# Optimization experiments

Hardware: AMD Instinct MI355X
Metric: run time of the kernel (lower is better)

The kernel has to match this reference:

```python
import jax, jax.numpy as jnp
import numpy as np

EPS = 1e-08
LAMBDA_SIM = 1.0
LAMBDA_SPARSITY = 0.001
B, D, K = 8192, 4096, 64


def setup_inputs() -> dict:
    key = jax.random.key(0)
    k1, k2, k3, k4, k5 = jax.random.split(key, 5)
    labels = jax.random.randint(k1, (B,), 0, K)
    hard_class_probs = jax.nn.one_hot(labels, K, dtype=jnp.float32)  # [B,K] hard one-hot
    return {
        "hard_class_probs": hard_class_probs,
        "masked_activations_1b": jax.random.normal(k2, (B, D), dtype=jnp.float32),
        "masked_activations_8b": jax.random.normal(k3, (B, D), dtype=jnp.float32),
        "mask_1b": jax.random.uniform(k4, (B, D), dtype=jnp.float32),
        "mask_8b": jax.random.uniform(k5, (B, D), dtype=jnp.float32),
    }


def _classwise_pairwise_cossim(acts, hard_class_probs):
    # F.normalize(p=2, dim=-1, eps=EPS): x / max(||x||, eps)
    norms = jnp.sqrt(jnp.sum(acts * acts, axis=-1, keepdims=True))
    norm_acts = acts / jnp.maximum(norms, EPS)                      # [B,D]
    S = norm_acts @ norm_acts.T                                      # [B,B] gram of unit vectors
    diag = jnp.sum(norm_acts * norm_acts, axis=-1)                   # [B] (== diag(S))
    M = (hard_class_probs > 0.5).astype(acts.dtype)                  # [B,K] hard membership
    n = jnp.sum(M, axis=0)                                           # [K] class counts
    SM = S @ M                                                       # [B,K]
    mSm = jnp.sum(M * SM, axis=0)                                    # [K] sum_{i,j in class} S_ij
    sum_diag = M.T @ diag                                            # [K]
    pair_sum = 0.5 * (mSm - sum_diag)                                # sum over i<j pairs
    n_pairs = 0.5 * n * (n - 1.0)
    valid = n >= 2.0
    per_class_mean = jnp.where(valid, pair_sum / jnp.maximum(n_pairs, 1.0), 0.0)
    n_valid = jnp.sum(valid.astype(acts.dtype))
    return jnp.where(n_valid > 0, jnp.sum(per_class_mean) / jnp.maximum(n_valid, 1.0), 0.0)


def _binary_entropy(p):
    p = jnp.clip(p, EPS, 1.0 - EPS)
    return jnp.mean(-(p * jnp.log(p) + (1.0 - p) * jnp.log(1.0 - p)))


def _combined_loss(hard_class_probs, masked_activations, mask):
    sim_loss = -_classwise_pairwise_cossim(masked_activations, hard_class_probs)
    sparsity_loss = _binary_entropy(mask)
    total = LAMBDA_SIM * sim_loss + LAMBDA_SPARSITY * sparsity_loss
    return total, sim_loss, sparsity_loss


def reference(hard_class_probs, masked_activations_1b, masked_activations_8b, mask_1b, mask_8b):
    loss_1b, sim_1b, sp_1b = _combined_loss(hard_class_probs, masked_activations_1b, mask_1b)
    loss_8b, sim_8b, sp_8b = _combined_loss(hard_class_probs, masked_activations_8b, mask_8b)
    total_loss = loss_1b + loss_8b
    return (total_loss, sim_1b, sim_8b, sp_1b, sp_8b)
```

## Files before the change

### kernel.cpp

```cpp
#include <hip/hip_runtime.h>
#include <math.h>

#define B_ 8192
#define D_ 4096
#define K_ 64
#define EPSF 1e-8f
#define NSPLIT 4
#define LN2F 0.69314718056f

#define ENT_GRID 2048
#define ENT_BLOCK 256

typedef float f32x4 __attribute__((ext_vector_type(4)));


__device__ __forceinline__ float wave_reduce_f(float v) {
#pragma unroll
  for (int o = 32; o > 0; o >>= 1) v += __shfl_down(v, o);
  return v;
}


__global__ void k_init(int* __restrict__ counts) {
  if (threadIdx.x < K_) counts[threadIdx.x] = 0;
}

__global__ void k_labels(const float* __restrict__ probs, int* __restrict__ labels,
                         int* __restrict__ counts, int* __restrict__ rowlist) {
  int row = blockIdx.x * 4 + (threadIdx.x >> 6);
  int lane = threadIdx.x & 63;
  float p = probs[(size_t)row * K_ + lane];
  unsigned long long m = __ballot(p > 0.5f);
  if (lane == 0) {
    int k = __ffsll(m) - 1;
    if (k >= 0) {
      labels[row] = k;
      int pos = atomicAdd(&counts[k], 1);
      rowlist[k * B_ + pos] = row;
    }
  }
}

__device__ __forceinline__ float ent1(float p) {
  p = fminf(fmaxf(p, EPSF), 1.0f - EPSF);
  float q = 1.0f - p;
  float lp = __builtin_amdgcn_logf(p);
  float lq = __builtin_amdgcn_logf(fmaxf(q, 1e-38f));
  return -(p * lp + q * lq);
}

__device__ __forceinline__ float ent4(f32x4 v) {
  return ent1(v.x) + ent1(v.y) + ent1(v.z) + ent1(v.w);
}

__global__ __launch_bounds__(ENT_BLOCK) void k_entropy(const f32x4* __restrict__ m1,
                                                       const f32x4* __restrict__ m8,
                                                       double* __restrict__ entpart) {
  __shared__ float lds[8];
  const int NTH = ENT_GRID * ENT_BLOCK;
  int tid = blockIdx.x * ENT_BLOCK + threadIdx.x;
  float s1 = 0.f, s8 = 0.f;
#pragma unroll
  for (int o = 0; o < 4; ++o) {
    f32x4 a[4], b[4];
#pragma unroll
    for (int j = 0; j < 4; ++j) {
      int idx = tid + (o * 4 + j) * NTH;
      a[j] = __builtin_nontemporal_load(&m1[idx]);
      b[j] = __builtin_nontemporal_load(&m8[idx]);
    }
#pragma unroll
    for (int j = 0; j < 4; ++j) {
      s1 += ent4(a[j]);
      s8 += ent4(b[j]);
    }
  }
  s1 = wave_reduce_f(s1);
  s8 = wave_reduce_f(s8);
  int wid = threadIdx.x >> 6;
  if ((threadIdx.x & 63) == 0) { lds[wid] = s1; lds[4 + wid] = s8; }
  __syncthreads();
  if (threadIdx.x == 0) {
    float t1 = lds[0] + lds[1] + lds[2] + lds[3];
    float t8 = lds[4] + lds[5] + lds[6] + lds[7];
    entpart[blockIdx.x]            = (double)(t1 * LN2F);
    entpart[ENT_GRID + blockIdx.x] = (double)(t8 * LN2F);
  }
}

__global__ __launch_bounds__(256) void k_norms(const float* __restrict__ acts,
                                               float* __restrict__ wout,
                                               float* __restrict__ diagout) {
  __shared__ float lds[4];
  int row = blockIdx.x;
  const float4* rp = (const float4*)(acts + (size_t)row * D_);
  int t = threadIdx.x;
  float4 v0 = rp[t];
  float4 v1 = rp[t + 256];
  float4 v2 = rp[t + 512];
  float4 v3 = rp[t + 768];
  float s = v0.x * v0.x + v0.y * v0.y + v0.z * v0.z + v0.w * v0.w;
  s += v1.x * v1.x + v1.y * v1.y + v1.z * v1.z + v1.w * v1.w;
  s += v2.x * v2.x + v2.y * v2.y + v2.z * v2.z + v2.w * v2.w;
  s += v3.x * v3.x + v3.y * v3.y + v3.z * v3.z + v3.w * v3.w;
  s = wave_reduce_f(s);
  int wid = t >> 6;
  if ((t & 63) == 0) lds[wid] = s;
  __syncthreads();
  if (t == 0) {
    s = lds[0] + lds[1] + lds[2] + lds[3];
    float n = sqrtf(s);
    float w = 1.0f / fmaxf(n, EPSF);
    wout[row] = w;
    diagout[row] = s * w * w;
  }
}

__global__ __launch_bounds__(256) void k_classsum(const float* __restrict__ acts,
                                                  const int* __restrict__ counts,
                                                  const int* __restrict__ rowlist,
                                                  const float* __restrict__ warr,
                                                  float* __restrict__ Cpart) {
  int bid = blockIdx.x;
  int k = bid & 63;
  int cc = (bid >> 6) & 3;
  int split = bid >> 8;
  int cnt = counts[k];
  int beg = (cnt * split) / NSPLIT;
  int end = (cnt * (split + 1)) / NSPLIT;
  int t = threadIdx.x;
  int col = cc * 1024 + 4 * t;
  const int* rl = rowlist + k * B_;
  float4 acc0 = make_float4(0.f, 0.f, 0.f, 0.f);
  float4 acc1 = make_float4(0.f, 0.f, 0.f, 0.f);
  int r = beg;
  for (; r + 2 <= end; r += 2) {
    int row0 = rl[r];
    int row1 = rl[r + 1];
    float w0 = warr[row0];
    float w1 = warr[row1];
    float4 v0 = *(const float4*)(acts + (size_t)row0 * D_ + col);
    float4 v1 = *(const float4*)(acts + (size_t)row1 * D_ + col);
    acc0.x += w0 * v0.x; acc0.y += w0 * v0.y; acc0.z += w0 * v0.z; acc0.w += w0 * v0.w;
    acc1.x += w1 * v1.x; acc1.y += w1 * v1.y; acc1.z += w1 * v1.z; acc1.w += w1 * v1.w;
  }
  if (r < end) {
    int row0 = rl[r];
    float w0 = warr[row0];
    float4 v0 = *(const float4*)(acts + (size_t)row0 * D_ + col);
    acc0.x += w0 * v0.x; acc0.y += w0 * v0.y; acc0.z += w0 * v0.z; acc0.w += w0 * v0.w;
  }
  acc0.x += acc1.x; acc0.y += acc1.y; acc0.z += acc1.z; acc0.w += acc1.w;
  *(float4*)(Cpart + ((size_t)split * K_ + k) * D_ + col) = acc0;
}

__global__ void k_msm(const float* __restrict__ Cpart, float* __restrict__ mSm) {
  __shared__ float lds[4];
  int k = blockIdx.x;
  int t = threadIdx.x;
  float s = 0.f;
#pragma unroll
  for (int j = 0; j < D_ / 256; ++j) {
    size_t base = (size_t)k * D_ + t + 256 * j;
    float c = Cpart[base] + Cpart[(size_t)K_ * D_ + base] + Cpart[2ull * K_ * D_ + base] +
              Cpart[3ull * K_ * D_ + base];
    s += c * c;
  }
  s = wave_reduce_f(s);
  int wid = t >> 6;
  if ((t & 63) == 0) lds[wid] = s;
  __syncthreads();
  if (t == 0) mSm[k] = lds[0] + lds[1] + lds[2] + lds[3];
}

__global__ void k_final(const double* __restrict__ entpart, const int* __restrict__ labels,
                        const int* __restrict__ counts, const float* __restrict__ diag1,
                        const float* __restrict__ diag8, const float* __restrict__ mSm1,
                        const float* __restrict__ mSm8, float* __restrict__ out) {
  __shared__ float sd1[K_], sd8[K_];
  __shared__ double dl[8];
  int t = threadIdx.x;
  if (t < K_) { sd1[t] = 0.f; sd8[t] = 0.f; }
  __syncthreads();
  for (int r = t; r < B_; r += 256) {
    int k = labels[r];
    atomicAdd(&sd1[k], diag1[r]);
    atomicAdd(&sd8[k], diag8[r]);
  }
  double e1 = 0.0, e8 = 0.0;
  for (int i = t; i < 2048; i += 256) {
    e1 += entpart[i];
    e8 += entpart[2048 + i];
  }
#pragma unroll
  for (int o = 32; o > 0; o >>= 1) {
    e1 += __shfl_down(e1, o);
    e8 += __shfl_down(e8, o);
  }
  int wid = t >> 6;
  if ((t & 63) == 0) { dl[wid] = e1; dl[4 + wid] = e8; }
  __syncthreads();
  float pcm1 = 0.f, pcm8 = 0.f, valid = 0.f;
  if (t < K_) {
    float n = (float)counts[t];
    bool v = (n >= 2.0f);
    float np = fmaxf(0.5f * n * (n - 1.0f), 1.0f);
    valid = v ? 1.0f : 0.f;
    pcm1 = v ? 0.5f * (mSm1[t] - sd1[t]) / np : 0.f;
    pcm8 = v ? 0.5f * (mSm8[t] - sd8[t]) / np : 0.f;
  }
#pragma unroll
  for (int o = 32; o > 0; o >>= 1) {
    pcm1 += __shfl_down(pcm1, o);
    pcm8 += __shfl_down(pcm8, o);
    valid += __shfl_down(valid, o);
  }
  if (t == 0) {
    double etot1 = dl[0] + dl[1] + dl[2] + dl[3];
    double etot8 = dl[4] + dl[5] + dl[6] + dl[7];
    float sp1 = (float)(etot1 / (double)((long long)B_ * D_));
    float sp8 = (float)(etot8 / (double)((long long)B_ * D_));
    float cs1 = (valid > 0.f) ? pcm1 / fmaxf(valid, 1.0f) : 0.f;
    float cs8 = (valid > 0.f) ? pcm8 / fmaxf(valid, 1.0f) : 0.f;
    float sim1 = -cs1, sim8 = -cs8;
    out[0] = sim1 + sim8 + 0.001f * (sp1 + sp8);
    out[1] = sim1;
    out[2] = sim8;
    out[3] = sp1;
    out[4] = sp8;
  }
}


extern "C" void kernel_launch(void* const* d_in, const int* in_sizes, int n_in,
                              void* d_out, int out_size, void* d_ws, size_t ws_size,
                              hipStream_t stream) {
  const float* probs = (const float*)d_in[0];
  const float* a1 = (const float*)d_in[1];
  const float* a8 = (const float*)d_in[2];
  const float* m1 = (const float*)d_in[3];
  const float* m8 = (const float*)d_in[4];
  float* out = (float*)d_out;
  char* ws = (char*)d_ws;

  double* entpart = (double*)(ws + 0);
  int* labels = (int*)(ws + 32768);
  int* counts = (int*)(ws + 65536);
  float* mSm = (float*)(ws + 65792);
  float* warr = (float*)(ws + 66560);
  float* diag = (float*)(ws + 132096);
  int* rowlist = (int*)(ws + 197632);
  float* Cpart = (float*)(ws + 2294784);

  k_init<<<1, 64, 0, stream>>>(counts);
  k_labels<<<B_ / 4, 256, 0, stream>>>(probs, labels, counts, rowlist);
  k_entropy<<<ENT_GRID, ENT_BLOCK, 0, stream>>>((const f32x4*)m1, (const f32x4*)m8, entpart);
  k_norms<<<B_, 256, 0, stream>>>(a1, warr, diag);
  k_classsum<<<K_ * 4 * NSPLIT, 256, 0, stream>>>(a1, counts, rowlist, warr, Cpart);
  k_msm<<<K_, 256, 0, stream>>>(Cpart, mSm);
  k_norms<<<B_, 256, 0, stream>>>(a8, warr + B_, diag + B_);
  k_classsum<<<K_ * 4 * NSPLIT, 256, 0, stream>>>(a8, counts, rowlist, warr + B_, Cpart);
  k_msm<<<K_, 256, 0, stream>>>(Cpart, mSm + K_);
  k_final<<<1, 256, 0, stream>>>(entpart, labels, counts, diag, diag + B_, mSm, mSm + K_, out);
}
```

Before: 206.4 us.

## Widen class-sum split, parallelize msm, fold diag into norms, reorder entropy

Raises the class-sum row split from 4 to 8 when the workspace allows, unrolls the class-sum loop to four independent accumulators, and switches its row reads to nontemporal loads. The msm reduction moves from one block per class to four blocks per class, with the final kernel summing the partials. Per-class diagonal sums are now accumulated with global atomics in k_norms, which removes the serial pass over all rows in k_final. The entropy kernel is moved to run after the similarity kernels, possibly so the activations stay cache-resident between the norm and class-sum passes. The trade-off is more Cpart memory and global atomic contention on 64 addresses.

After: 256.7 us. 24.3% more time.

```diff
diff --git a/kernel.cpp b/kernel.cpp
--- a/kernel.cpp
+++ b/kernel.cpp
@@ -5,7 +5,6 @@
 #define D_ 4096
 #define K_ 64
 #define EPSF 1e-8f
-#define NSPLIT 4
 #define LN2F 0.69314718056f
 
 #define ENT_GRID 2048
@@ -21,8 +20,8 @@
 }
 
 
-__global__ void k_init(int* __restrict__ counts) {
-  if (threadIdx.x < K_) counts[threadIdx.x] = 0;
+__global__ void k_init(int* __restrict__ z) {
+  if (threadIdx.x < 192) z[threadIdx.x] = 0;
 }
 
 __global__ void k_labels(const float* __restrict__ probs, int* __restrict__ labels,
@@ -41,56 +40,10 @@
   }
 }
 
-__device__ __forceinline__ float ent1(float p) {
-  p = fminf(fmaxf(p, EPSF), 1.0f - EPSF);
-  float q = 1.0f - p;
-  float lp = __builtin_amdgcn_logf(p);
-  float lq = __builtin_amdgcn_logf(fmaxf(q, 1e-38f));
-  return -(p * lp + q * lq);
-}
-
-__device__ __forceinline__ float ent4(f32x4 v) {
-  return ent1(v.x) + ent1(v.y) + ent1(v.z) + ent1(v.w);
-}
-
-__global__ __launch_bounds__(ENT_BLOCK) void k_entropy(const f32x4* __restrict__ m1,
-                                                       const f32x4* __restrict__ m8,
-                                                       double* __restrict__ entpart) {
-  __shared__ float lds[8];
-  const int NTH = ENT_GRID * ENT_BLOCK;
-  int tid = blockIdx.x * ENT_BLOCK + threadIdx.x;
-  float s1 = 0.f, s8 = 0.f;
-#pragma unroll
-  for (int o = 0; o < 4; ++o) {
-    f32x4 a[4], b[4];
-#pragma unroll
-    for (int j = 0; j < 4; ++j) {
-      int idx = tid + (o * 4 + j) * NTH;
-      a[j] = __builtin_nontemporal_load(&m1[idx]);
-      b[j] = __builtin_nontemporal_load(&m8[idx]);
-    }
-#pragma unroll
-    for (int j = 0; j < 4; ++j) {
-      s1 += ent4(a[j]);
-      s8 += ent4(b[j]);
-    }
-  }
-  s1 = wave_reduce_f(s1);
-  s8 = wave_reduce_f(s8);
-  int wid = threadIdx.x >> 6;
-  if ((threadIdx.x & 63) == 0) { lds[wid] = s1; lds[4 + wid] = s8; }
-  __syncthreads();
-  if (threadIdx.x == 0) {
-    float t1 = lds[0] + lds[1] + lds[2] + lds[3];
-    float t8 = lds[4] + lds[5] + lds[6] + lds[7];
-    entpart[blockIdx.x]            = (double)(t1 * LN2F);
-    entpart[ENT_GRID + blockIdx.x] = (double)(t8 * LN2F);
-  }
-}
-
 __global__ __launch_bounds__(256) void k_norms(const float* __restrict__ acts,
+                                               const int* __restrict__ labels,
                                                float* __restrict__ wout,
-                                               float* __restrict__ diagout) {
+                                               float* __restrict__ sd) {
   __shared__ float lds[4];
   int row = blockIdx.x;
   const float4* rp = (const float4*)(acts + (size_t)row * D_);
@@ -112,7 +65,7 @@
     float n = sqrtf(s);
     float w = 1.0f / fmaxf(n, EPSF);
     wout[row] = w;
-    diagout[row] = s * w * w;
+    atomicAdd(&sd[labels[row]], s * w * w);
   }
 }
 
@@ -120,77 +73,115 @@
                                                   const int* __restrict__ counts,
                                                   const int* __restrict__ rowlist,
                                                   const float* __restrict__ warr,
-                                                  float* __restrict__ Cpart) {
+                                                  float* __restrict__ Cpart, int nsplit) {
   int bid = blockIdx.x;
   int k = bid & 63;
   int cc = (bid >> 6) & 3;
   int split = bid >> 8;
   int cnt = counts[k];
-  int beg = (cnt * split) / NSPLIT;
-  int end = (cnt * (split + 1)) / NSPLIT;
+  int beg = (cnt * split) / nsplit;
+  int end = (cnt * (split + 1)) / nsplit;
   int t = threadIdx.x;
   int col = cc * 1024 + 4 * t;
   const int* rl = rowlist + k * B_;
-  float4 acc0 = make_float4(0.f, 0.f, 0.f, 0.f);
-  float4 acc1 = make_float4(0.f, 0.f, 0.f, 0.f);
+  f32x4 acc0 = 0.f, acc1 = 0.f, acc2 = 0.f, acc3 = 0.f;
   int r = beg;
-  for (; r + 2 <= end; r += 2) {
-    int row0 = rl[r];
-    int row1 = rl[r + 1];
-    float w0 = warr[row0];
-    float w1 = warr[row1];
-    float4 v0 = *(const float4*)(acts + (size_t)row0 * D_ + col);
-    float4 v1 = *(const float4*)(acts + (size_t)row1 * D_ + col);
-    acc0.x += w0 * v0.x; acc0.y += w0 * v0.y; acc0.z += w0 * v0.z; acc0.w += w0 * v0.w;
-    acc1.x += w1 * v1.x; acc1.y += w1 * v1.y; acc1.z += w1 * v1.z; acc1.w += w1 * v1.w;
-  }
-  if (r < end) {
+  for (; r + 4 <= end; r += 4) {
+    int row0 = rl[r], row1 = rl[r + 1], row2 = rl[r + 2], row3 = rl[r + 3];
+    float w0 = warr[row0], w1 = warr[row1], w2 = warr[row2], w3 = warr[row3];
+    f32x4 v0 = __builtin_nontemporal_load((const f32x4*)(acts + (size_t)row0 * D_ + col));
+    f32x4 v1 = __builtin_nontemporal_load((const f32x4*)(acts + (size_t)row1 * D_ + col));
+    f32x4 v2 = __builtin_nontemporal_load((const f32x4*)(acts + (size_t)row2 * D_ + col));
+    f32x4 v3 = __builtin_nontemporal_load((const f32x4*)(acts + (size_t)row3 * D_ + col));
+    acc0 += w0 * v0;
+    acc1 += w1 * v1;
+    acc2 += w2 * v2;
+    acc3 += w3 * v3;
+  }
+  for (; r < end; ++r) {
     int row0 = rl[r];
     float w0 = warr[row0];
-    float4 v0 = *(const float4*)(acts + (size_t)row0 * D_ + col);
-    acc0.x += w0 * v0.x; acc0.y += w0 * v0.y; acc0.z += w0 * v0.z; acc0.w += w0 * v0.w;
-  }
-  acc0.x += acc1.x; acc0.y += acc1.y; acc0.z += acc1.z; acc0.w += acc1.w;
-  *(float4*)(Cpart + ((size_t)split * K_ + k) * D_ + col) = acc0;
-}
-
-__global__ void k_msm(const float* __restrict__ Cpart, float* __restrict__ mSm) {
+    f32x4 v0 = __builtin_nontemporal_load((const f32x4*)(acts + (size_t)row0 * D_ + col));
+    acc0 += w0 * v0;
+  }
+  acc0 += acc1 + acc2 + acc3;
+  *(f32x4*)(Cpart + ((size_t)split * K_ + k) * D_ + col) = acc0;
+}
+
+__global__ void k_msm(const float* __restrict__ Cpart, int nsplit, float* __restrict__ msp) {
   __shared__ float lds[4];
-  int k = blockIdx.x;
-  int t = threadIdx.x;
-  float s = 0.f;
-#pragma unroll
-  for (int j = 0; j < D_ / 256; ++j) {
-    size_t base = (size_t)k * D_ + t + 256 * j;
-    float c = Cpart[base] + Cpart[(size_t)K_ * D_ + base] + Cpart[2ull * K_ * D_ + base] +
-              Cpart[3ull * K_ * D_ + base];
-    s += c * c;
-  }
-  s = wave_reduce_f(s);
+  int k = blockIdx.x >> 2;
+  int q = blockIdx.x & 3;
+  int t = threadIdx.x;
+  int col = q * 1024 + 4 * t;
+  f32x4 c = 0.f;
+  for (int s = 0; s < nsplit; ++s)
+    c += *(const f32x4*)(Cpart + ((size_t)s * K_ + k) * D_ + col);
+  float sq = c.x * c.x + c.y * c.y + c.z * c.z + c.w * c.w;
+  sq = wave_reduce_f(sq);
   int wid = t >> 6;
-  if ((t & 63) == 0) lds[wid] = s;
-  __syncthreads();
-  if (t == 0) mSm[k] = lds[0] + lds[1] + lds[2] + lds[3];
-}
-
-__global__ void k_final(const double* __restrict__ entpart, const int* __restrict__ labels,
-                        const int* __restrict__ counts, const float* __restrict__ diag1,
-                        const float* __restrict__ diag8, const float* __restrict__ mSm1,
-                        const float* __restrict__ mSm8, float* __restrict__ out) {
-  __shared__ float sd1[K_], sd8[K_];
+  if ((t & 63) == 0) lds[wid] = sq;
+  __syncthreads();
+  if (t == 0) msp[blockIdx.x] = lds[0] + lds[1] + lds[2] + lds[3];
+}
+
+__device__ __forceinline__ float ent1(float p) {
+  p = fminf(fmaxf(p, EPSF), 1.0f - EPSF);
+  float q = 1.0f - p;
+  float lp = __builtin_amdgcn_logf(p);
+  float lq = __builtin_amdgcn_logf(fmaxf(q, 1e-38f));
+  return -(p * lp + q * lq);
+}
+
+__device__ __forceinline__ float ent4(f32x4 v) {
+  return ent1(v.x) + ent1(v.y) + ent1(v.z) + ent1(v.w);
+}
+
+__global__ __launch_bounds__(ENT_BLOCK) void k_entropy(const f32x4* __restrict__ m1,
+                                                       const f32x4* __restrict__ m8,
+                                                       double* __restrict__ entpart) {
+  __shared__ float lds[8];
+  const int NTH = ENT_GRID * ENT_BLOCK;
+  int tid = blockIdx.x * ENT_BLOCK + threadIdx.x;
+  float s1 = 0.f, s8 = 0.f;
+#pragma unroll
+  for (int o = 0; o < 4; ++o) {
+    f32x4 a[4], b[4];
+#pragma unroll
+    for (int j = 0; j < 4; ++j) {
+      int idx = tid + (o * 4 + j) * NTH;
+      a[j] = __builtin_nontemporal_load(&m1[idx]);
+      b[j] = __builtin_nontemporal_load(&m8[idx]);
+    }
+#pragma unroll
+    for (int j = 0; j < 4; ++j) {
+      s1 += ent4(a[j]);
+      s8 += ent4(b[j]);
+    }
+  }
+  s1 = wave_reduce_f(s1);
+  s8 = wave_reduce_f(s8);
+  int wid = threadIdx.x >> 6;
+  if ((threadIdx.x & 63) == 0) { lds[wid] = s1; lds[4 + wid] = s8; }
+  __syncthreads();
+  if (threadIdx.x == 0) {
+    float t1 = lds[0] + lds[1] + lds[2] + lds[3];
+    float t8 = lds[4] + lds[5] + lds[6] + lds[7];
+    entpart[blockIdx.x]            = (double)(t1 * LN2F);
+    entpart[ENT_GRID + blockIdx.x] = (double)(t8 * LN2F);
+  }
+}
+
+__global__ void k_final(const double* __restrict__ entpart, const int* __restrict__ counts,
+                        const float* __restrict__ sd1, const float* __restrict__ sd8,
+                        const float* __restrict__ msp1, const float* __restrict__ msp8,
+                        float* __restrict__ out) {
   __shared__ double dl[8];
   int t = threadIdx.x;
-  if (t < K_) { sd1[t] = 0.f; sd8[t] = 0.f; }
-  __syncthreads();
-  for (int r = t; r < B_; r += 256) {
-    int k = labels[r];
-    atomicAdd(&sd1[k], diag1[r]);
-    atomicAdd(&sd8[k], diag8[r]);
-  }
   double e1 = 0.0, e8 = 0.0;
-  for (int i = t; i < 2048; i += 256) {
+  for (int i = t; i < ENT_GRID; i += 256) {
     e1 += entpart[i];
-    e8 += entpart[2048 + i];
+    e8 += entpart[ENT_GRID + i];
   }
 #pragma unroll
   for (int o = 32; o > 0; o >>= 1) {
@@ -202,12 +193,14 @@
   __syncthreads();
   float pcm1 = 0.f, pcm8 = 0.f, valid = 0.f;
   if (t < K_) {
+    float mSm1 = msp1[t * 4] + msp1[t * 4 + 1] + msp1[t * 4 + 2] + msp1[t * 4 + 3];
+    float mSm8 = msp8[t * 4] + msp8[t * 4 + 1] + msp8[t * 4 + 2] + msp8[t * 4 + 3];
     float n = (float)counts[t];
     bool v = (n >= 2.0f);
     float np = fmaxf(0.5f * n * (n - 1.0f), 1.0f);
     valid = v ? 1.0f : 0.f;
-    pcm1 = v ? 0.5f * (mSm1[t] - sd1[t]) / np : 0.f;
-    pcm8 = v ? 0.5f * (mSm8[t] - sd8[t]) / np : 0.f;
+    pcm1 = v ? 0.5f * (mSm1 - sd1[t]) / np : 0.f;
+    pcm8 = v ? 0.5f * (mSm8 - sd8[t]) / np : 0.f;
   }
 #pragma unroll
   for (int o = 32; o > 0; o >>= 1) {
@@ -246,20 +239,25 @@
   double* entpart = (double*)(ws + 0);
   int* labels = (int*)(ws + 32768);
   int* counts = (int*)(ws + 65536);
-  float* mSm = (float*)(ws + 65792);
-  float* warr = (float*)(ws + 66560);
-  float* diag = (float*)(ws + 132096);
-  int* rowlist = (int*)(ws + 197632);
-  float* Cpart = (float*)(ws + 2294784);
-
-  k_init<<<1, 64, 0, stream>>>(counts);
+  float* sd1 = (float*)(ws + 65792);
+  float* sd8 = (float*)(ws + 66048);
+  float* msp1 = (float*)(ws + 66304);
+  float* msp8 = (float*)(ws + 67328);
+  float* warr1 = (float*)(ws + 69632);
+  float* warr8 = (float*)(ws + 102400);
+  int* rowlist = (int*)(ws + 135168);
+  float* Cpart = (float*)(ws + 2232320);
+
+  int nsplit = (ws_size >= (size_t)2232320 + 8u * 1024 * 1024 + 65536) ? 8 : 4;
+
+  k_init<<<1, 256, 0, stream>>>(counts);
   k_labels<<<B_ / 4, 256, 0, stream>>>(probs, labels, counts, rowlist);
-  k_entropy<<<ENT_GRID, ENT_BLOCK, 0, stream>>>((const f32x4*)m1, (const f32x4*)m8, entpart);
-  k_norms<<<B_, 256, 0, stream>>>(a1, warr, diag);
-  k_classsum<<<K_ * 4 * NSPLIT, 256, 0, stream>>>(a1, counts, rowlist, warr, Cpart);
-  k_msm<<<K_, 256, 0, stream>>>(Cpart, mSm);
-  k_norms<<<B_, 256, 0, stream>>>(a8, warr + B_, diag + B_);
-  k_classsum<<<K_ * 4 * NSPLIT, 256, 0, stream>>>(a8, counts, rowlist, warr + B_, Cpart);
-  k_msm<<<K_, 256, 0, stream>>>(Cpart, mSm + K_);
-  k_final<<<1, 256, 0, stream>>>(entpart, labels, counts, diag, diag + B_, mSm, mSm + K_, out);
-}
+  k_norms<<<B_, 256, 0, stream>>>(a1, labels, warr1, sd1);
+  k_classsum<<<256 * nsplit, 256, 0, stream>>>(a1, counts, rowlist, warr1, Cpart, nsplit);
+  k_msm<<<256, 256, 0, stream>>>(Cpart, nsplit, msp1);
+  k_norms<<<B_, 256, 0, stream>>>(a8, labels, warr8, sd8);
+  k_classsum<<<256 * nsplit, 256, 0, stream>>>(a8, counts, rowlist, warr8, Cpart, nsplit);
+  k_msm<<<256, 256, 0, stream>>>(Cpart, nsplit, msp8);
+  k_entropy<<<ENT_GRID, 256, 0, stream>>>((const f32x4*)m1, (const f32x4*)m8, entpart);
+  k_final<<<1, 256, 0, stream>>>(entpart, counts, sd1, sd8, msp1, msp8, out);
+}
```
